# Kernel tuning notes

Hardware: AMD Instinct MI355X
Metric: run time of the kernel (lower is better)

Reference implementation:

```python
import jax, jax.numpy as jnp
import numpy as np

N = 40000      # nodes
E = 640000     # edges (before self-loops)
F_IN = 32      # num_node_features
H = 8          # n_heads
C = 16         # hidden_channels
G = 1000       # graphs in batch
M = 256        # MLP_neurons
NEG_SLOPE = 0.2


def setup_inputs() -> dict:
    key = jax.random.key(0)
    ks = jax.random.split(key, 24)
    d = {}
    d["x"] = jax.random.normal(ks[0], (N, F_IN), jnp.float32)
    d["edge_index"] = jax.random.randint(ks[1], (2, E), 0, N, dtype=jnp.int32)
    d["batch"] = jnp.sort(jax.random.randint(ks[2], (N,), 0, G, dtype=jnp.int32))
    dims = [F_IN, H * C, H * C]
    k = 3
    for i in range(3):
        fin = dims[i]
        s = 1.0 / np.sqrt(fin)
        d[f"W{i}"] = jax.random.normal(ks[k], (fin, H * C), jnp.float32) * s; k += 1
        d[f"b{i}"] = jnp.zeros((H * C,), jnp.float32)
        d[f"as{i}"] = jax.random.normal(ks[k], (H, C), jnp.float32) * (1.0 / np.sqrt(C)); k += 1
        d[f"ad{i}"] = jax.random.normal(ks[k], (H, C), jnp.float32) * (1.0 / np.sqrt(C)); k += 1
    d["fW0"] = jax.random.normal(ks[k], (H * C, M), jnp.float32) * (1.0 / np.sqrt(H * C)); k += 1
    d["fb0"] = jnp.zeros((M,), jnp.float32)
    d["fW1"] = jax.random.normal(ks[k], (M, M), jnp.float32) * (1.0 / np.sqrt(M)); k += 1
    d["fb1"] = jnp.zeros((M,), jnp.float32)
    d["oW"] = jax.random.normal(ks[k], (M, 2), jnp.float32) * (1.0 / np.sqrt(M)); k += 1
    d["ob"] = jnp.zeros((2,), jnp.float32)
    return d


def _gat_layer(x, W, b, a_src, a_dst, src, dst):
    # x: [N, Fin] -> h: [N, H, C]
    h = (x @ W).reshape(N, H, C)
    al_src = jnp.einsum('nhc,hc->nh', h, a_src)   # [N, H]
    al_dst = jnp.einsum('nhc,hc->nh', h, a_dst)   # [N, H]
    # edge-wise attention logits (gather), LeakyReLU
    e = jax.nn.leaky_relu(al_src[src] + al_dst[dst], NEG_SLOPE)  # [E', H]
    # softmax over incoming edges of each dst node
    emax = jax.ops.segment_max(e, dst, num_segments=N)           # [N, H]
    ex = jnp.exp(e - emax[dst])
    denom = jax.ops.segment_sum(ex, dst, num_segments=N)         # [N, H]
    alpha = ex / denom[dst]
    # weighted scatter-aggregation of source features
    out = jax.ops.segment_sum(alpha[:, :, None] * h[src], dst, num_segments=N)  # [N, H, C]
    return out.reshape(N, H * C) + b


def reference(x, edge_index, batch, W0, b0, as0, ad0, W1, b1, as1, ad1,
              W2, b2, as2, ad2, fW0, fb0, fW1, fb1, oW, ob):
    # PyG GATConv adds self-loops by default
    loops = jnp.arange(N, dtype=edge_index.dtype)
    src = jnp.concatenate([edge_index[0], loops])
    dst = jnp.concatenate([edge_index[1], loops])
    h = x
    for (W, b, a_s, a_d) in ((W0, b0, as0, ad0), (W1, b1, as1, ad1), (W2, b2, as2, ad2)):
        h = jax.nn.relu(_gat_layer(h, W, b, a_s, a_d, src, dst))
    # global mean pool per graph
    sums = jax.ops.segment_sum(h, batch, num_segments=G)                    # [G, H*C]
    cnts = jax.ops.segment_sum(jnp.ones((N,), h.dtype), batch, num_segments=G)
    g = sums / jnp.maximum(cnts, 1.0)[:, None]
    # MLP head (dropout is identity in eval mode)
    g = jax.nn.relu(g @ fW0 + fb0)
    g = jax.nn.relu(g @ fW1 + fb1)
    return g @ oW + ob
```

## Files before the change

### kernel.cpp

```cpp
#include <hip/hip_runtime.h>
#include <hip/hip_fp16.h>
#include <math.h>

#define NN 40000
#define EE 640000
#define EP 680000
#define FIN0 32
#define HC 128
#define GG 1000
#define MM 256
#define PROJ0_BLOCKS (NN / 64)
#define NB 333
#define NBIN 157
#define HSIZE (NBIN * NB)
#define SCAN2_BLOCKS ((HSIZE + 255) / 256)
#define PADH 136

typedef _Float16 f16x8 __attribute__((ext_vector_type(8)));
typedef float f32x4 __attribute__((ext_vector_type(4)));


__global__ __launch_bounds__(256) void prep_kernel(const float* __restrict__ X,
                                                   const float* __restrict__ W0,
                                                   const float* __restrict__ a_src,
                                                   const float* __restrict__ a_dst,
                                                   __half* __restrict__ H2,
                                                   float* __restrict__ als,
                                                   float* __restrict__ ald,
                                                   const int* __restrict__ ei,
                                                   int* __restrict__ hist,
                                                   const float* __restrict__ W1,
                                                   const float* __restrict__ W2,
                                                   __half* __restrict__ Wt1,
                                                   __half* __restrict__ Wt2) {
    int t = threadIdx.x;
    int b = blockIdx.x;
    if (b >= PROJ0_BLOCKS && b < PROJ0_BLOCKS + NB) {
        __shared__ int hb[NBIN];
        int blk = b - PROJ0_BLOCKS;
        for (int i = t; i < NBIN; i += 256) hb[i] = 0;
        __syncthreads();
        int base = blk * 2048 + t;
#pragma unroll
        for (int k = 0; k < 8; k++) {
            int idx = base + k * 256;
            if (idx < EP) {
                int d = (idx < EE) ? ei[EE + idx] : (idx - EE);
                atomicAdd(&hb[d >> 8], 1);
            }
        }
        __syncthreads();
        for (int i = t; i < NBIN; i += 256) hist[i * NB + blk] = hb[i];
        return;
    }
    if (b >= PROJ0_BLOCKS + NB) {
        int l = b - (PROJ0_BLOCKS + NB);
        const float* Wsrc = (l == 0) ? W1 : W2;
        __half* Wd = (l == 0) ? Wt1 : Wt2;
#pragma unroll 8
        for (int r = 0; r < 64; r++) {
            int idx = r * 256 + t;
            int k = idx >> 7, c = idx & 127;
            Wd[c * 128 + k] = __float2half(Wsrc[idx]);
        }
        return;
    }
    __shared__ float xs[32][68];
    __shared__ float ws[32][128];
    int node0 = b * 64;
    int nt = t & 15;
    int ct = t >> 4;
    float acc[4][8];
#pragma unroll
    for (int i = 0; i < 4; i++)
#pragma unroll
        for (int j = 0; j < 8; j++) acc[i][j] = 0.f;
#pragma unroll
    for (int r = 0; r < 8; r++) {
        int idx = r * 256 + t;
        int n = idx >> 5, k = idx & 31;
        xs[k][n] = X[(node0 + n) * FIN0 + k];
    }
#pragma unroll
    for (int r = 0; r < 16; r++) {
        int idx = r * 256 + t;
        int k = idx >> 7, c = idx & 127;
        ws[k][c] = W0[k * 128 + c];
    }
    __syncthreads();
#pragma unroll
    for (int k = 0; k < 32; k++) {
        const float4 xv = *(const float4*)(&xs[k][4 * nt]);
        const float4 wa = *(const float4*)(&ws[k][8 * ct]);
        const float4 wb = *(const float4*)(&ws[k][8 * ct + 4]);
        float xr[4] = {xv.x, xv.y, xv.z, xv.w};
        float wr[8] = {wa.x, wa.y, wa.z, wa.w, wb.x, wb.y, wb.z, wb.w};
#pragma unroll
        for (int i = 0; i < 4; i++)
#pragma unroll
            for (int j = 0; j < 8; j++) acc[i][j] = fmaf(xr[i], wr[j], acc[i][j]);
    }
#pragma unroll
    for (int i = 0; i < 4; i++) {
        int n = node0 + 4 * nt + i;
        __half2 p0 = __floats2half2_rn(acc[i][0], acc[i][1]);
        __half2 p1 = __floats2half2_rn(acc[i][2], acc[i][3]);
        __half2 p2 = __floats2half2_rn(acc[i][4], acc[i][5]);
        __half2 p3 = __floats2half2_rn(acc[i][6], acc[i][7]);
        uint4 pk;
        pk.x = *(unsigned*)&p0; pk.y = *(unsigned*)&p1;
        pk.z = *(unsigned*)&p2; pk.w = *(unsigned*)&p3;
        *(uint4*)(&H2[(size_t)n * HC + 8 * ct]) = pk;
    }
    float sa[4] = {0.f, 0.f, 0.f, 0.f}, da[4] = {0.f, 0.f, 0.f, 0.f};
#pragma unroll
    for (int j = 0; j < 8; j++) {
        float av = a_src[ct * 8 + j];
        float dv = a_dst[ct * 8 + j];
#pragma unroll
        for (int i = 0; i < 4; i++) {
            sa[i] = fmaf(acc[i][j], av, sa[i]);
            da[i] = fmaf(acc[i][j], dv, da[i]);
        }
    }
#pragma unroll
    for (int i = 0; i < 4; i++) {
        sa[i] += __shfl_xor(sa[i], 16);
        da[i] += __shfl_xor(da[i], 16);
    }
    if ((ct & 1) == 0) {
        int head = ct >> 1;
#pragma unroll
        for (int i = 0; i < 4; i++) {
            int n = node0 + 4 * nt + i;
            als[n * 8 + head] = sa[i];
            ald[n * 8 + head] = da[i];
        }
    }
}


__global__ __launch_bounds__(256) void scan_partial2(const int* __restrict__ hist,
                                                     int* __restrict__ part) {
    int b = blockIdx.x, t = threadIdx.x;
    int i = b * 256 + t;
    int v = (i < HSIZE) ? hist[i] : 0;
#pragma unroll
    for (int d = 1; d < 64; d <<= 1) v += __shfl_xor(v, d);
    __shared__ int ws[4];
    if ((t & 63) == 0) ws[t >> 6] = v;
    __syncthreads();
    if (t == 0) part[b] = ws[0] + ws[1] + ws[2] + ws[3];
}

__global__ __launch_bounds__(256) void scan_final2(const int* __restrict__ hist,
                                                   const int* __restrict__ part,
                                                   int* __restrict__ base) {
    int b = blockIdx.x, t = threadIdx.x;
    __shared__ int sbase;
    if (t < 64) {
        int s = 0;
        for (int l = t; l < b; l += 64) s += part[l];
#pragma unroll
        for (int d = 1; d < 64; d <<= 1) s += __shfl_xor(s, d);
        if (t == 0) sbase = s;
    }
    int i = b * 256 + t;
    int v = (i < HSIZE) ? hist[i] : 0;
    __shared__ int tmp[256];
    tmp[t] = v;
    __syncthreads();
    for (int st = 1; st < 256; st <<= 1) {
        int add = (t >= st) ? tmp[t - st] : 0;
        __syncthreads();
        tmp[t] += add;
        __syncthreads();
    }
    int excl = tmp[t] - v + sbase;
    if (i < HSIZE) base[i] = excl;
}


__global__ __launch_bounds__(256) void radix_c1(const int* __restrict__ ei,
                                                const int* __restrict__ base,
                                                unsigned* __restrict__ tmp) {
    __shared__ int lbase[NBIN];
    __shared__ int lcnt[NBIN];
    int t = threadIdx.x, blk = blockIdx.x;
    for (int i = t; i < NBIN; i += 256) { lbase[i] = base[i * NB + blk]; lcnt[i] = 0; }
    __syncthreads();
    int start = blk * 2048 + t;
#pragma unroll
    for (int k = 0; k < 8; k++) {
        int idx = start + k * 256;
        if (idx < EP) {
            int s, d;
            if (idx < EE) { s = ei[idx]; d = ei[EE + idx]; } else { s = idx - EE; d = s; }
            int bin = d >> 8;
            int r = atomicAdd(&lcnt[bin], 1);
            tmp[lbase[bin] + r] = ((unsigned)d << 16) | (unsigned)s;
        }
    }
}


__global__ __launch_bounds__(256) void radix_p2(const unsigned* __restrict__ tmp,
                                                const int* __restrict__ base,
                                                int* __restrict__ esrc,
                                                int* __restrict__ offs) {
    __shared__ int cnt[256];
    __shared__ int sc[256];
    int t = threadIdx.x, k = blockIdx.x;
    int bb = base[k * NB];
    int be = (k == NBIN - 1) ? EP : base[(k + 1) * NB];
    cnt[t] = 0;
    __syncthreads();
    for (int e = bb + t; e < be; e += 256) {
        unsigned v = tmp[e];
        atomicAdd(&cnt[(v >> 16) & 255], 1);
    }
    __syncthreads();
    int myc = cnt[t];
    sc[t] = myc;
    __syncthreads();
    for (int st = 1; st < 256; st <<= 1) {
        int add = (t >= st) ? sc[t - st] : 0;
        __syncthreads();
        sc[t] += add;
        __syncthreads();
    }
    int ex = sc[t] - myc;
    int d = k * 256 + t;
    if (d < NN) offs[d] = bb + ex;
    if (k == NBIN - 1 && t == 0) offs[NN] = EP;
    __syncthreads();
    cnt[t] = ex;
    __syncthreads();
    for (int e = bb + t; e < be; e += 256) {
        unsigned v = tmp[e];
        int d0 = (v >> 16) & 255;
        int r = atomicAdd(&cnt[d0], 1);
        esrc[bb + r] = (int)(v & 0xFFFFu);
    }
}


__global__ __launch_bounds__(256) void proj_mfma(const __half* __restrict__ Bin,
                                                 const __half* __restrict__ Wt,
                                                 const float* __restrict__ a_src,
                                                 const float* __restrict__ a_dst,
                                                 __half* __restrict__ H2,
                                                 float* __restrict__ als,
                                                 float* __restrict__ ald) {
    __shared__ __half As[64 * PADH];
    __shared__ __half Ws[128 * PADH];
    int t = threadIdx.x;
    int node0 = blockIdx.x * 64;
    {
        int n = t >> 2, kk = (t & 3) * 32;
        const uint4* src = (const uint4*)(&Bin[(size_t)(node0 + n) * 128 + kk]);
        uint4 v0 = src[0];
        uint4 v1 = src[1];
        uint4 v2 = src[2];
        uint4 v3 = src[3];
        uint4* dst = (uint4*)(&As[n * PADH + kk]);
        dst[0] = v0; dst[1] = v1; dst[2] = v2; dst[3] = v3;
    }
#pragma unroll
    for (int r = 0; r < 8; r++) {
        int idx = r * 256 + t;
        int c = idx >> 4;
        int kk = (idx & 15) * 8;
        uint4 v = *(const uint4*)(&Wt[c * 128 + kk]);
        *(uint4*)(&Ws[c * PADH + kk]) = v;
    }
    __syncthreads();
    int w = t >> 6, l = t & 63;
    int lr = l & 15, lg = l >> 4;
    f32x4 acc[8];
    f32x4 z4 = {0.f, 0.f, 0.f, 0.f};
#pragma unroll
    for (int n = 0; n < 8; n++) acc[n] = z4;
    const __half* arow = &As[(16 * w + lr) * PADH + lg * 8];
#pragma unroll
    for (int ks = 0; ks < 4; ks++) {
        f16x8 af = *(const f16x8*)(arow + 32 * ks);
#pragma unroll
        for (int n = 0; n < 8; n++) {
            f16x8 bf = *(const f16x8*)(&Ws[(16 * n + lr) * PADH + lg * 8 + 32 * ks]);
            acc[n] = __builtin_amdgcn_mfma_f32_16x16x32_f16(af, bf, acc[n], 0, 0, 0);
        }
    }
#pragma unroll
    for (int n = 0; n < 8; n++)
#pragma unroll
        for (int j = 0; j < 4; j++)
            As[(16 * w + lg * 4 + j) * PADH + 16 * n + lr] = __float2half(acc[n][j]);
    __syncthreads();
    {
        int n = t >> 2, kk = (t & 3) * 32;
        const uint4* src = (const uint4*)(&As[n * PADH + kk]);
        uint4 v0 = src[0];
        uint4 v1 = src[1];
        uint4 v2 = src[2];
        uint4 v3 = src[3];
        uint4* dst = (uint4*)(&H2[(size_t)(node0 + n) * 128 + kk]);
        dst[0] = v0; dst[1] = v1; dst[2] = v2; dst[3] = v3;
    }
    {
        int nt = t & 15, ct = t >> 4;
        float av[8], dv[8];
#pragma unroll
        for (int j = 0; j < 8; j++) { av[j] = a_src[ct * 8 + j]; dv[j] = a_dst[ct * 8 + j]; }
        float sa[4], da[4];
#pragma unroll
        for (int i = 0; i < 4; i++) {
            uint4 hv = *(const uint4*)(&As[(4 * nt + i) * PADH + 8 * ct]);
            __half2 h0 = *(__half2*)&hv.x;
            __half2 h1 = *(__half2*)&hv.y;
            __half2 h2 = *(__half2*)&hv.z;
            __half2 h3 = *(__half2*)&hv.w;
            float2 f0 = __half22float2(h0);
            float2 f1 = __half22float2(h1);
            float2 f2 = __half22float2(h2);
            float2 f3 = __half22float2(h3);
            sa[i] = f0.x * av[0] + f0.y * av[1] + f1.x * av[2] + f1.y * av[3] +
                    f2.x * av[4] + f2.y * av[5] + f3.x * av[6] + f3.y * av[7];
            da[i] = f0.x * dv[0] + f0.y * dv[1] + f1.x * dv[2] + f1.y * dv[3] +
                    f2.x * dv[4] + f2.y * dv[5] + f3.x * dv[6] + f3.y * dv[7];
        }
#pragma unroll
        for (int i = 0; i < 4; i++) {
            sa[i] += __shfl_xor(sa[i], 16);
            da[i] += __shfl_xor(da[i], 16);
        }
        if ((ct & 1) == 0) {
            int head = ct >> 1;
#pragma unroll
            for (int i = 0; i < 4; i++) {
                int n = node0 + 4 * nt + i;
                als[n * 8 + head] = sa[i];
                ald[n * 8 + head] = da[i];
            }
        }
    }
}


template <bool HALF_OUT>
__global__ __launch_bounds__(256) void agg_kernel(const __half* __restrict__ H2,
                                                  const float* __restrict__ als,
                                                  const float* __restrict__ ald,
                                                  const int* __restrict__ offs,
                                                  const int* __restrict__ esrc,
                                                  const float* __restrict__ bias,
                                                  float* __restrict__ OUT,
                                                  __half* __restrict__ OUT2) {
    int t = threadIdx.x;
    int n = blockIdx.x * 4 + (t >> 6);
    int t6 = t & 63;
    int c8 = t6 & 15;
    int slot = (t6 >> 4) & 3;
    int hd = c8 >> 1;
    int beg = offs[n], end = offs[n + 1];
    float ad = ald[n * 8 + hd];
    float acc[8] = {0.f, 0.f, 0.f, 0.f, 0.f, 0.f, 0.f, 0.f};
    float denom = 0.f;
    const float4* H4 = (const float4*)H2;

    int p = beg + slot;
    int s_cur = 0; float al_cur = 0.f;
    if (p < end) {
        s_cur = esrc[p];
        al_cur = als[s_cur * 8 + hd];
    }
#pragma unroll 2
    while (p < end) {
        int pn = p + 4;
        int s_nxt = 0;
        if (pn < end) s_nxt = esrc[pn];
        float x = al_cur + ad;
        x = (x > 0.f) ? x : 0.2f * x;
        float w = __expf(x);
        float4 r = H4[(size_t)s_cur * 16 + c8];
        float al_nxt = 0.f;
        if (pn < end) al_nxt = als[s_nxt * 8 + hd];
        __half2 h0 = *(__half2*)&r.x;
        __half2 h1 = *(__half2*)&r.y;
        __half2 h2 = *(__half2*)&r.z;
        __half2 h3 = *(__half2*)&r.w;
        float2 f0 = __half22float2(h0);
        float2 f1 = __half22float2(h1);
        float2 f2 = __half22float2(h2);
        float2 f3 = __half22float2(h3);
        acc[0] = fmaf(w, f0.x, acc[0]); acc[1] = fmaf(w, f0.y, acc[1]);
        acc[2] = fmaf(w, f1.x, acc[2]); acc[3] = fmaf(w, f1.y, acc[3]);
        acc[4] = fmaf(w, f2.x, acc[4]); acc[5] = fmaf(w, f2.y, acc[5]);
        acc[6] = fmaf(w, f3.x, acc[6]); acc[7] = fmaf(w, f3.y, acc[7]);
        denom += w;
        s_cur = s_nxt; al_cur = al_nxt;
        p = pn;
    }
#pragma unroll
    for (int j = 0; j < 8; j++) {
        acc[j] += __shfl_xor(acc[j], 16);
        acc[j] += __shfl_xor(acc[j], 32);
    }
    denom += __shfl_xor(denom, 16);
    denom += __shfl_xor(denom, 32);
    if (slot == 0 && t6 < 16) {
        float inv = 1.0f / denom;
        const float4 ba = ((const float4*)bias)[2 * c8];
        const float4 bb = ((const float4*)bias)[2 * c8 + 1];
        float o0 = fmaxf(fmaf(acc[0], inv, ba.x), 0.f);
        float o1 = fmaxf(fmaf(acc[1], inv, ba.y), 0.f);
        float o2 = fmaxf(fmaf(acc[2], inv, ba.z), 0.f);
        float o3 = fmaxf(fmaf(acc[3], inv, ba.w), 0.f);
        float o4 = fmaxf(fmaf(acc[4], inv, bb.x), 0.f);
        float o5 = fmaxf(fmaf(acc[5], inv, bb.y), 0.f);
        float o6 = fmaxf(fmaf(acc[6], inv, bb.z), 0.f);
        float o7 = fmaxf(fmaf(acc[7], inv, bb.w), 0.f);
        if (HALF_OUT) {
            __half2 q0 = __floats2half2_rn(o0, o1);
            __half2 q1 = __floats2half2_rn(o2, o3);
            __half2 q2 = __floats2half2_rn(o4, o5);
            __half2 q3 = __floats2half2_rn(o6, o7);
            uint4 pk;
            pk.x = *(unsigned*)&q0; pk.y = *(unsigned*)&q1;
            pk.z = *(unsigned*)&q2; pk.w = *(unsigned*)&q3;
            ((uint4*)OUT2)[(size_t)n * 16 + c8] = pk;
        } else {
            float4 v0, v1;
            v0.x = o0; v0.y = o1; v0.z = o2; v0.w = o3;
            v1.x = o4; v1.y = o5; v1.z = o6; v1.w = o7;
            ((float4*)OUT)[(size_t)n * 32 + 2 * c8]     = v0;
            ((float4*)OUT)[(size_t)n * 32 + 2 * c8 + 1] = v1;
        }
    }
}


__global__ __launch_bounds__(256) void mlp_fused(const float* __restrict__ B,
                                                 const int* __restrict__ batch,
                                                 const float* __restrict__ fW0,
                                                 const float* __restrict__ fb0,
                                                 const float* __restrict__ fW1,
                                                 const float* __restrict__ fb1,
                                                 const float* __restrict__ oW,
                                                 const float* __restrict__ ob,
                                                 float* __restrict__ out) {
    __shared__ int lo[3];
    __shared__ float rows[2][128];
    __shared__ float g1s[2][256];
    __shared__ float g2s[2][256];
    int t = threadIdx.x;
    int g0 = blockIdx.x * 2;
    if (t < 3) {
        int target = g0 + t;
        int a = 0, b = NN;
        while (a < b) { int mid = (a + b) >> 1; if (batch[mid] < target) a = mid + 1; else b = mid; }
        lo[t] = a;
    }
    __syncthreads();
    {
        int j = t >> 7, c = t & 127;
        int s0 = lo[j], s1 = lo[j + 1];
        float s = 0.f;
        float p0 = 0.f, p1 = 0.f, p2 = 0.f, p3 = 0.f;
        int n = s0;
        for (; n + 3 < s1; n += 4) {
            p0 += B[(size_t)n * 128 + c];
            p1 += B[(size_t)(n + 1) * 128 + c];
            p2 += B[(size_t)(n + 2) * 128 + c];
            p3 += B[(size_t)(n + 3) * 128 + c];
        }
        for (; n < s1; n++) s += B[(size_t)n * 128 + c];
        s += (p0 + p1) + (p2 + p3);
        rows[j][c] = s / fmaxf((float)(s1 - s0), 1.0f);
    }
    __syncthreads();
    float a0 = 0.f, a1 = 0.f;
#pragma unroll 8
    for (int k = 0; k < 128; k++) {
        float w = fW0[k * 256 + t];
        a0 = fmaf(rows[0][k], w, a0);
        a1 = fmaf(rows[1][k], w, a1);
    }
    float b0v = fb0[t];
    g1s[0][t] = fmaxf(a0 + b0v, 0.f);
    g1s[1][t] = fmaxf(a1 + b0v, 0.f);
    __syncthreads();
    a0 = 0.f; a1 = 0.f;
#pragma unroll 8
    for (int k = 0; k < 256; k++) {
        float w = fW1[k * 256 + t];
        a0 = fmaf(g1s[0][k], w, a0);
        a1 = fmaf(g1s[1][k], w, a1);
    }
    float b1v = fb1[t];
    g2s[0][t] = fmaxf(a0 + b1v, 0.f);
    g2s[1][t] = fmaxf(a1 + b1v, 0.f);
    __syncthreads();
    if (t < 64) {
        int jj = t >> 5, l = t & 31;
        float p0 = 0.f, p1 = 0.f;
#pragma unroll
        for (int k = l; k < 256; k += 32) {
            float v = g2s[jj][k];
            p0 = fmaf(v, oW[k * 2 + 0], p0);
            p1 = fmaf(v, oW[k * 2 + 1], p1);
        }
#pragma unroll
        for (int d = 1; d < 32; d <<= 1) {
            p0 += __shfl_xor(p0, d);
            p1 += __shfl_xor(p1, d);
        }
        if (l == 0) {
            out[(g0 + jj) * 2 + 0] = p0 + ob[0];
            out[(g0 + jj) * 2 + 1] = p1 + ob[1];
        }
    }
}


extern "C" void kernel_launch(void* const* d_in, const int* in_sizes, int n_in,
                              void* d_out, int out_size, void* d_ws, size_t ws_size,
                              hipStream_t stream) {
    const float* x    = (const float*)d_in[0];
    const int* ei     = (const int*)d_in[1];
    const int* batch  = (const int*)d_in[2];
    const float* W[3]   = {(const float*)d_in[3], (const float*)d_in[7],  (const float*)d_in[11]};
    const float* bs[3]  = {(const float*)d_in[4], (const float*)d_in[8],  (const float*)d_in[12]};
    const float* asr[3] = {(const float*)d_in[5], (const float*)d_in[9],  (const float*)d_in[13]};
    const float* adt[3] = {(const float*)d_in[6], (const float*)d_in[10], (const float*)d_in[14]};
    const float* fW0 = (const float*)d_in[15];
    const float* fb0 = (const float*)d_in[16];
    const float* fW1 = (const float*)d_in[17];
    const float* fb1 = (const float*)d_in[18];
    const float* oW  = (const float*)d_in[19];
    const float* ob  = (const float*)d_in[20];
    float* out = (float*)d_out;

    char* base_ws = (char*)d_ws;
    size_t off = 0;
    auto alloc = [&](size_t bytes) -> void* {
        void* p = base_ws + off;
        off += (bytes + 255) & ~(size_t)255;
        return p;
    };
    int* hist     = (int*)alloc((size_t)HSIZE * 4);
    int* sbase    = (int*)alloc((size_t)HSIZE * 4);
    int* part     = (int*)alloc((size_t)SCAN2_BLOCKS * 4);
    unsigned* tmp = (unsigned*)alloc((size_t)EP * 4);
    int* offs     = (int*)alloc((size_t)(NN + 1) * 4);
    int* esrc     = (int*)alloc((size_t)EP * 4);
    __half* H2  = (__half*)alloc((size_t)NN * HC * 2);
    float* B    = (float*)alloc((size_t)NN * HC * 4);
    __half* B2  = (__half*)alloc((size_t)NN * HC * 2);
    float* als  = (float*)alloc((size_t)NN * 8 * 4);
    float* ald  = (float*)alloc((size_t)NN * 8 * 4);
    __half* Wt1 = (__half*)alloc((size_t)HC * HC * 2);
    __half* Wt2 = (__half*)alloc((size_t)HC * HC * 2);

    prep_kernel<<<PROJ0_BLOCKS + NB + 2, 256, 0, stream>>>(
        x, W[0], asr[0], adt[0], H2, als, ald, ei, hist, W[1], W[2], Wt1, Wt2);
    scan_partial2<<<SCAN2_BLOCKS, 256, 0, stream>>>(hist, part);
    scan_final2<<<SCAN2_BLOCKS, 256, 0, stream>>>(hist, part, sbase);
    radix_c1<<<NB, 256, 0, stream>>>(ei, sbase, tmp);
    radix_p2<<<NBIN, 256, 0, stream>>>(tmp, sbase, esrc, offs);

    agg_kernel<true><<<NN / 4, 256, 0, stream>>>(H2, als, ald, offs, esrc, bs[0], nullptr, B2);
    proj_mfma<<<PROJ0_BLOCKS, 256, 0, stream>>>(B2, Wt1, asr[1], adt[1], H2, als, ald);
    agg_kernel<true><<<NN / 4, 256, 0, stream>>>(H2, als, ald, offs, esrc, bs[1], nullptr, B2);
    proj_mfma<<<PROJ0_BLOCKS, 256, 0, stream>>>(B2, Wt2, asr[2], adt[2], H2, als, ald);
    agg_kernel<false><<<NN / 4, 256, 0, stream>>>(H2, als, ald, offs, esrc, bs[2], B, nullptr);

    mlp_fused<<<GG / 2, 256, 0, stream>>>(B, batch, fW0, fb0, fW1, fb1, oW, ob, out);
}
```

Before: 288.2 us.

## Fold histogram scan into radix scatter kernels, dropping two scan launches

The two-kernel global prefix scan over the bin-by-block histogram is removed. Each radix_c1 block now recomputes, in a transposed block-major layout, the per-bin totals and its own per-bin prefix by reading the whole histogram, followed by a shared-memory scan. radix_p2 likewise recomputes bin totals and scans to find its range. This cuts two kernel launches and a global round trip, at the cost of every block reading the full histogram of about 52K ints redundantly.

```diff
diff --git a/kernel.cpp b/kernel.cpp
--- a/kernel.cpp
+++ b/kernel.cpp
@@ -12,8 +12,7 @@
 #define PROJ0_BLOCKS (NN / 64)
 #define NB 333
 #define NBIN 157
-#define HSIZE (NBIN * NB)
-#define SCAN2_BLOCKS ((HSIZE + 255) / 256)
+#define HSIZE (NB * NBIN)
 #define PADH 136
 
 typedef _Float16 f16x8 __attribute__((ext_vector_type(8)));
@@ -50,7 +49,7 @@
             }
         }
         __syncthreads();
-        for (int i = t; i < NBIN; i += 256) hist[i * NB + blk] = hb[i];
+        for (int i = t; i < NBIN; i += 256) hist[blk * NBIN + i] = hb[i];
         return;
     }
     if (b >= PROJ0_BLOCKS + NB) {
@@ -140,54 +139,31 @@
 }
 
 
-__global__ __launch_bounds__(256) void scan_partial2(const int* __restrict__ hist,
-                                                     int* __restrict__ part) {
-    int b = blockIdx.x, t = threadIdx.x;
-    int i = b * 256 + t;
-    int v = (i < HSIZE) ? hist[i] : 0;
-#pragma unroll
-    for (int d = 1; d < 64; d <<= 1) v += __shfl_xor(v, d);
-    __shared__ int ws[4];
-    if ((t & 63) == 0) ws[t >> 6] = v;
-    __syncthreads();
-    if (t == 0) part[b] = ws[0] + ws[1] + ws[2] + ws[3];
-}
-
-__global__ __launch_bounds__(256) void scan_final2(const int* __restrict__ hist,
-                                                   const int* __restrict__ part,
-                                                   int* __restrict__ base) {
-    int b = blockIdx.x, t = threadIdx.x;
-    __shared__ int sbase;
-    if (t < 64) {
-        int s = 0;
-        for (int l = t; l < b; l += 64) s += part[l];
-#pragma unroll
-        for (int d = 1; d < 64; d <<= 1) s += __shfl_xor(s, d);
-        if (t == 0) sbase = s;
-    }
-    int i = b * 256 + t;
-    int v = (i < HSIZE) ? hist[i] : 0;
-    __shared__ int tmp[256];
-    tmp[t] = v;
-    __syncthreads();
-    for (int st = 1; st < 256; st <<= 1) {
-        int add = (t >= st) ? tmp[t - st] : 0;
-        __syncthreads();
-        tmp[t] += add;
-        __syncthreads();
-    }
-    int excl = tmp[t] - v + sbase;
-    if (i < HSIZE) base[i] = excl;
-}
-
-
 __global__ __launch_bounds__(256) void radix_c1(const int* __restrict__ ei,
-                                                const int* __restrict__ base,
+                                                const int* __restrict__ hist,
                                                 unsigned* __restrict__ tmp) {
     __shared__ int lbase[NBIN];
     __shared__ int lcnt[NBIN];
+    __shared__ int sc[256];
     int t = threadIdx.x, blk = blockIdx.x;
-    for (int i = t; i < NBIN; i += 256) { lbase[i] = base[i * NB + blk]; lcnt[i] = 0; }
+    int tot = 0, pref = 0;
+    if (t < NBIN) {
+#pragma unroll 4
+        for (int b = 0; b < NB; b++) {
+            int h = hist[b * NBIN + t];
+            tot += h;
+            pref += (b < blk) ? h : 0;
+        }
+    }
+    sc[t] = tot;
+    __syncthreads();
+    for (int st = 1; st < 256; st <<= 1) {
+        int add = (t >= st) ? sc[t - st] : 0;
+        __syncthreads();
+        sc[t] += add;
+        __syncthreads();
+    }
+    if (t < NBIN) { lbase[t] = (sc[t] - tot) + pref; lcnt[t] = 0; }
     __syncthreads();
     int start = blk * 2048 + t;
 #pragma unroll
@@ -205,14 +181,29 @@
 
 
 __global__ __launch_bounds__(256) void radix_p2(const unsigned* __restrict__ tmp,
-                                                const int* __restrict__ base,
+                                                const int* __restrict__ hist,
                                                 int* __restrict__ esrc,
                                                 int* __restrict__ offs) {
     __shared__ int cnt[256];
     __shared__ int sc[256];
+    __shared__ int bbs, bes;
     int t = threadIdx.x, k = blockIdx.x;
-    int bb = base[k * NB];
-    int be = (k == NBIN - 1) ? EP : base[(k + 1) * NB];
+    int tot = 0;
+    if (t < NBIN) {
+#pragma unroll 4
+        for (int b = 0; b < NB; b++) tot += hist[b * NBIN + t];
+    }
+    sc[t] = tot;
+    __syncthreads();
+    for (int st = 1; st < 256; st <<= 1) {
+        int add = (t >= st) ? sc[t - st] : 0;
+        __syncthreads();
+        sc[t] += add;
+        __syncthreads();
+    }
+    if (t == k) { bbs = sc[t] - tot; bes = sc[t]; }
+    __syncthreads();
+    int bb = bbs, be = bes;
     cnt[t] = 0;
     __syncthreads();
     for (int e = bb + t; e < be; e += 256) {
@@ -549,8 +540,6 @@
         return p;
     };
     int* hist     = (int*)alloc((size_t)HSIZE * 4);
-    int* sbase    = (int*)alloc((size_t)HSIZE * 4);
-    int* part     = (int*)alloc((size_t)SCAN2_BLOCKS * 4);
     unsigned* tmp = (unsigned*)alloc((size_t)EP * 4);
     int* offs     = (int*)alloc((size_t)(NN + 1) * 4);
     int* esrc     = (int*)alloc((size_t)EP * 4);
@@ -564,10 +553,8 @@
 
     prep_kernel<<<PROJ0_BLOCKS + NB + 2, 256, 0, stream>>>(
         x, W[0], asr[0], adt[0], H2, als, ald, ei, hist, W[1], W[2], Wt1, Wt2);
-    scan_partial2<<<SCAN2_BLOCKS, 256, 0, stream>>>(hist, part);
-    scan_final2<<<SCAN2_BLOCKS, 256, 0, stream>>>(hist, part, sbase);
-    radix_c1<<<NB, 256, 0, stream>>>(ei, sbase, tmp);
-    radix_p2<<<NBIN, 256, 0, stream>>>(tmp, sbase, esrc, offs);
+    radix_c1<<<NB, 256, 0, stream>>>(ei, hist, tmp);
+    radix_p2<<<NBIN, 256, 0, stream>>>(tmp, hist, esrc, offs);
 
     agg_kernel<true><<<NN / 4, 256, 0, stream>>>(H2, als, ald, offs, esrc, bs[0], nullptr, B2);
     proj_mfma<<<PROJ0_BLOCKS, 256, 0, stream>>>(B2, Wt1, asr[1], adt[1], H2, als, ald);
```

New measurement: 319.1 us. 1.11x slower.
